# Kernel tuning notes

Hardware: AMD Instinct MI355X
Metric: run time of the kernel (lower is better)

## Reference

```python
import jax, jax.numpy as jnp
import numpy as np
import math

D_MODEL = 1024
NUM_HEADS = 16
D_FF = 4096
LN_EPS = 1e-5


def _layer_norm(x, gamma, beta):
    mu = jnp.mean(x, axis=-1, keepdims=True)
    var = jnp.mean(jnp.square(x - mu), axis=-1, keepdims=True)
    return (x - mu) / jnp.sqrt(var + LN_EPS) * gamma + beta


def setup_inputs() -> dict:
    key = jax.random.key(0)
    ks = jax.random.split(key, 16)
    S, B, D, F = 2048, 2, D_MODEL, D_FF
    sc = 0.02
    inp = {
        "x": jax.random.normal(ks[0], (S, B, D), dtype=jnp.float32),
        "Wq": jax.random.normal(ks[1], (D, D), dtype=jnp.float32) * sc,
        "bq": jnp.zeros((D,), jnp.float32),
        "Wk": jax.random.normal(ks[2], (D, D), dtype=jnp.float32) * sc,
        "bk": jnp.zeros((D,), jnp.float32),
        "Wv": jax.random.normal(ks[3], (D, D), dtype=jnp.float32) * sc,
        "bv": jnp.zeros((D,), jnp.float32),
        "Wo": jax.random.normal(ks[4], (D, D), dtype=jnp.float32) * sc,
        "bo": jnp.zeros((D,), jnp.float32),
        "g1": jnp.ones((D,), jnp.float32),
        "b1": jnp.zeros((D,), jnp.float32),
        "W1": jax.random.normal(ks[5], (D, F), dtype=jnp.float32) * sc,
        "bb1": jnp.zeros((F,), jnp.float32),
        "W2": jax.random.normal(ks[6], (F, D), dtype=jnp.float32) * sc,
        "bb2": jnp.zeros((D,), jnp.float32),
        "g2": jnp.ones((D,), jnp.float32),
        "b2": jnp.zeros((D,), jnp.float32),
    }
    return inp


def reference(x, Wq, bq, Wk, bk, Wv, bv, Wo, bo, g1, b1, W1, bb1, W2, bb2, g2, b2):
    # x: [S, B, D] (seq-first, matching the torch module)
    S, B, D = x.shape
    H = NUM_HEADS
    dh = D // H

    def split_(t):  # [S, B, D] -> [B*H, S, dh]  (same as view + transpose in torch)
        return jnp.swapaxes(t.reshape(S, B * H, dh), 0, 1)

    q = split_(x @ Wq + bq)
    k = split_(x @ Wk + bk)
    v = split_(x @ Wv + bv)

    # naive bmm -> softmax -> bmm attention (full [B*H, S, S] scores)
    scores = jnp.einsum("nsd,ntd->nst", q / math.sqrt(dh), k)
    attn = jax.nn.softmax(scores, axis=-1)
    o = jnp.einsum("nst,ntd->nsd", attn, v)  # [B*H, S, dh]
    o = jnp.swapaxes(o, 0, 1).reshape(S, B, D) @ Wo + bo

    x1 = _layer_norm(x + o, g1, b1)
    ff = jax.nn.relu(x1 @ W1 + bb1) @ W2 + bb2
    return _layer_norm(x1 + ff, g2, b2)
```

## Files before the change

### kernel.cpp

```cpp
#include <hip/hip_runtime.h>
#include <hip/hip_bf16.h>
#include <cstdint>

typedef __bf16 bf16_t;
typedef __attribute__((ext_vector_type(8))) __bf16 bf16x8;
typedef __attribute__((ext_vector_type(4))) __bf16 bf16x4;
typedef __attribute__((ext_vector_type(2))) __bf16 bf16x2;
typedef __attribute__((ext_vector_type(4))) float f32x4;

#define GLOBAL_AS __attribute__((address_space(1)))
#define LDS_AS __attribute__((address_space(3)))

__device__ __forceinline__ void lds_load16(void* lds, const void* g) {
    __builtin_amdgcn_global_load_lds((GLOBAL_AS void*)g, (LDS_AS void*)lds, 16, 0, 0);
}

__global__ __launch_bounds__(256) void prep_all(const float* __restrict__ x,
                                                const float* __restrict__ Wq,
                                                const float* __restrict__ Wk,
                                                const float* __restrict__ Wv,
                                                const float* __restrict__ Wo,
                                                const float* __restrict__ W1,
                                                const float* __restrict__ W2,
                                                const float* __restrict__ bq,
                                                const float* __restrict__ bk,
                                                const float* __restrict__ bv,
                                                bf16_t* __restrict__ xb,
                                                bf16_t* __restrict__ WqkvT,
                                                bf16_t* __restrict__ WoT,
                                                bf16_t* __restrict__ W1T,
                                                bf16_t* __restrict__ W2T,
                                                float* __restrict__ qkvb) {
    __shared__ float T[64][65];
    const int bid = blockIdx.x, tid = threadIdx.x;
    if (bid < 3072) {
        const float* W; bf16_t* WT; int Kd, Nd, lb;
        if (bid < 1024) {
            Kd = 1024; Nd = 1024; lb = bid & 255;
            const int w = bid >> 8;
            W  = (w == 0) ? Wq : (w == 1) ? Wk : (w == 2) ? Wv : Wo;
            WT = (w == 0) ? WqkvT : (w == 1) ? WqkvT + 1048576
               : (w == 2) ? WqkvT + 2097152 : WoT;
        } else if (bid < 2048) { W = W1; WT = W1T; Kd = 1024; Nd = 4096; lb = bid - 1024; }
        else                   { W = W2; WT = W2T; Kd = 4096; Nd = 1024; lb = bid - 2048; }
        const int nbk = Kd >> 6;
        const int bk = lb % nbk, bn = lb / nbk;
        const int k0 = bk << 6, n0 = bn << 6;
        #pragma unroll
        for (int rep = 0; rep < 4; ++rep) {
            int r = rep * 16 + (tid >> 4);
            int c = (tid & 15) * 4;
            float4 v = *(const float4*)(W + (size_t)(k0 + r) * Nd + n0 + c);
            T[r][c] = v.x; T[r][c + 1] = v.y; T[r][c + 2] = v.z; T[r][c + 3] = v.w;
        }
        __syncthreads();
        #pragma unroll
        for (int rep = 0; rep < 4; ++rep) {
            int r = rep * 16 + (tid >> 4);
            int c = (tid & 15) * 4;
            bf16x4 o;
            o[0] = (bf16_t)T[c][r]; o[1] = (bf16_t)T[c + 1][r];
            o[2] = (bf16_t)T[c + 2][r]; o[3] = (bf16_t)T[c + 3][r];
            *(bf16x4*)(WT + (size_t)(n0 + r) * Kd + k0 + c) = o;
        }
    } else if (bid < 7168) {
        const int i = (bid - 3072) * 256 + tid;
        float4 v = *(const float4*)(x + (size_t)i * 4);
        bf16x4 o;
        o[0] = (bf16_t)v.x; o[1] = (bf16_t)v.y; o[2] = (bf16_t)v.z; o[3] = (bf16_t)v.w;
        *(bf16x4*)(xb + (size_t)i * 4) = o;
    } else {
        const int i = (bid - 7168) * 256 + tid;
        if (i < 3072)
            qkvb[i] = (i < 1024) ? bq[i] : (i < 2048) ? bk[i - 1024] : bv[i - 2048];
    }
}

template <int OM, bool RELU>
__global__ __launch_bounds__(512, 2) void gemm256(const bf16_t* __restrict__ A,
                                                  const bf16_t* __restrict__ Bt,
                                                  const float* __restrict__ bias,
                                                  void* __restrict__ Cv,
                                                  int M, int N, int K,
                                                  int kc_len, int n_kc) {
    __shared__ alignas(16) bf16_t As[2][256 * 64];
    __shared__ alignas(16) bf16_t Bs[2][256 * 64];
    const int tid = threadIdx.x;
    const int wid = tid >> 6, lane = tid & 63;
    const int lr = lane & 15, lg = lane >> 4;
    const int wr = wid >> 2, wc = wid & 3;
    const int lrsw = (lr & 7) << 4;

    const int nbn = N >> 8;
    const int nbase = (M >> 8) * nbn;
    const int nwg = nbase * n_kc;
    int bid = blockIdx.x;
    int wg;
    if ((nwg & 7) == 0) { int q = nwg >> 3; wg = (bid & 7) * q + (bid >> 3); }
    else wg = bid;
    const int kc = wg / nbase;
    const int inner = wg - kc * nbase;
    const int bm = inner / nbn, bn = inner % nbn;

    f32x4 acc[8][4];
    #pragma unroll
    for (int i = 0; i < 8; ++i)
        #pragma unroll
        for (int j = 0; j < 4; ++j) acc[i][j] = f32x4{0.f, 0.f, 0.f, 0.f};

    const int srow = wid * 16 + (lane >> 3);
    const int colbyte = (((lane & 7) ^ (lane >> 3)) << 4);
    const char* gA = (const char*)(A + ((size_t)(bm * 256 + srow) * K + kc * kc_len)) + colbyte;
    const char* gB = (const char*)(Bt + ((size_t)(bn * 256 + srow) * K + kc * kc_len)) + colbyte;
    const size_t rs8 = (size_t)8 * K * 2;
    const size_t rs128 = (size_t)128 * K * 2;

    auto stA = [&](int b, int half, int kt) {
        char* d = (char*)As[b] + (half * 128 + wid * 16) * 128;
        const char* s = gA + (size_t)half * rs128 + (size_t)kt * 128;
        lds_load16(d, s);
        lds_load16(d + 1024, s + rs8);
    };
    auto stB = [&](int b, int half, int kt) {
        char* d = (char*)Bs[b] + (half * 128 + wid * 16) * 128;
        const char* s = gB + (size_t)half * rs128 + (size_t)kt * 128;
        lds_load16(d, s);
        lds_load16(d + 1024, s + rs8);
    };
    auto ldA = [&](int b, int m, int kk) {
        const int row = (m >> 2) * 128 + (m & 3) * 32 + wr * 16 + lr;
        return *(const bf16x8*)((const char*)As[b] + row * 128 + ((kk * 64 + lg * 16) ^ lrsw));
    };
    auto ldB = [&](int b, int n, int kk) {
        const int row = n * 64 + wc * 16 + lr;
        return *(const bf16x8*)((const char*)Bs[b] + row * 128 + ((kk * 64 + lg * 16) ^ lrsw));
    };

    const int NT = kc_len >> 6;
    stA(0, 0, 0); stB(0, 0, 0); stB(0, 1, 0); stA(0, 1, 0);
    asm volatile("s_waitcnt vmcnt(4)" ::: "memory");
    __builtin_amdgcn_s_barrier();

    bf16x8 afr[4][2], bfr[4][2];
    #pragma unroll 1
    for (int kt = 0; kt < NT; ++kt) {
        const int buf = kt & 1;
        const int ktn = (kt + 1 < NT) ? kt + 1 : kt;

        #pragma unroll
        for (int m = 0; m < 4; ++m) {
            afr[m][0] = ldA(buf, m, 0);
            afr[m][1] = ldA(buf, m, 1);
        }
        #pragma unroll
        for (int n = 0; n < 2; ++n) {
            bfr[n][0] = ldB(buf, n, 0);
            bfr[n][1] = ldB(buf, n, 1);
        }
        stA(buf ^ 1, 0, ktn);
        __builtin_amdgcn_s_barrier();
        __builtin_amdgcn_s_setprio(1);
        #pragma unroll
        for (int m = 0; m < 4; ++m)
            #pragma unroll
            for (int n = 0; n < 2; ++n) {
                acc[m][n] = __builtin_amdgcn_mfma_f32_16x16x32_bf16(afr[m][0], bfr[n][0], acc[m][n], 0, 0, 0);
                acc[m][n] = __builtin_amdgcn_mfma_f32_16x16x32_bf16(afr[m][1], bfr[n][1], acc[m][n], 0, 0, 0);
            }
        __builtin_amdgcn_s_setprio(0);
        asm volatile("s_waitcnt vmcnt(4)" ::: "memory");
        __builtin_amdgcn_s_barrier();

        #pragma unroll
        for (int n = 2; n < 4; ++n) {
            bfr[n][0] = ldB(buf, n, 0);
            bfr[n][1] = ldB(buf, n, 1);
        }
        stB(buf ^ 1, 0, ktn);
        __builtin_amdgcn_s_barrier();
        __builtin_amdgcn_s_setprio(1);
        #pragma unroll
        for (int m = 0; m < 4; ++m)
            #pragma unroll
            for (int n = 2; n < 4; ++n) {
                acc[m][n] = __builtin_amdgcn_mfma_f32_16x16x32_bf16(afr[m][0], bfr[n][0], acc[m][n], 0, 0, 0);
                acc[m][n] = __builtin_amdgcn_mfma_f32_16x16x32_bf16(afr[m][1], bfr[n][1], acc[m][n], 0, 0, 0);
            }
        __builtin_amdgcn_s_setprio(0);
        asm volatile("s_waitcnt vmcnt(4)" ::: "memory");
        __builtin_amdgcn_s_barrier();

        #pragma unroll
        for (int m = 0; m < 4; ++m) {
            afr[m][0] = ldA(buf, m + 4, 0);
            afr[m][1] = ldA(buf, m + 4, 1);
        }
        stB(buf ^ 1, 1, ktn);
        __builtin_amdgcn_s_barrier();
        __builtin_amdgcn_s_setprio(1);
        #pragma unroll
        for (int m = 0; m < 4; ++m)
            #pragma unroll
            for (int n = 0; n < 2; ++n) {
                acc[m + 4][n] = __builtin_amdgcn_mfma_f32_16x16x32_bf16(afr[m][0], bfr[n][0], acc[m + 4][n], 0, 0, 0);
                acc[m + 4][n] = __builtin_amdgcn_mfma_f32_16x16x32_bf16(afr[m][1], bfr[n][1], acc[m + 4][n], 0, 0, 0);
            }
        __builtin_amdgcn_s_setprio(0);
        __builtin_amdgcn_s_barrier();

        stA(buf ^ 1, 1, ktn);
        __builtin_amdgcn_s_barrier();
        __builtin_amdgcn_s_setprio(1);
        #pragma unroll
        for (int m = 0; m < 4; ++m)
            #pragma unroll
            for (int n = 2; n < 4; ++n) {
                acc[m + 4][n] = __builtin_amdgcn_mfma_f32_16x16x32_bf16(afr[m][0], bfr[n][0], acc[m + 4][n], 0, 0, 0);
                acc[m + 4][n] = __builtin_amdgcn_mfma_f32_16x16x32_bf16(afr[m][1], bfr[n][1], acc[m + 4][n], 0, 0, 0);
            }
        __builtin_amdgcn_s_setprio(0);
        asm volatile("s_waitcnt vmcnt(4)" ::: "memory");
        __builtin_amdgcn_s_barrier();
    }

    float* outf = (float*)Cv + (size_t)kc * M * N;
    bf16_t* outb = (bf16_t*)Cv + (size_t)kc * M * N;
    float bv[4];
    #pragma unroll
    for (int n = 0; n < 4; ++n) {
        const int c = (bn << 8) + n * 64 + wc * 16 + lr;
        bv[n] = (bias && kc == 0) ? bias[c] : 0.f;
    }
    #pragma unroll
    for (int m = 0; m < 8; ++m) {
        const int row0 = (bm << 8) + (m >> 2) * 128 + (m & 3) * 32 + wr * 16 + (lg << 2);
        #pragma unroll
        for (int n = 0; n < 4; ++n) {
            const int c = (bn << 8) + n * 64 + wc * 16 + lr;
            #pragma unroll
            for (int j = 0; j < 4; ++j) {
                float v = acc[m][n][j] + bv[n];
                if (RELU) v = fmaxf(v, 0.f);
                if (OM == 0)      ((bf16_t*)Cv)[(size_t)(row0 + j) * N + c] = (bf16_t)v;
                else if (OM == 1) outf[(size_t)(row0 + j) * N + c] = v;
                else              outb[(size_t)(row0 + j) * N + c] = (bf16_t)v;
            }
        }
    }
}

__global__ __launch_bounds__(256) void reshape_v(const bf16_t* __restrict__ QKV,
                                                 bf16_t* __restrict__ VT) {
    __shared__ alignas(16) bf16_t Vl[64][72];
    const int n = blockIdx.x >> 5, st = blockIdx.x & 31;
    const int b = n >> 4, h = n & 15;
    const int s0 = st << 6;
    const int tid = threadIdx.x;

    #pragma unroll
    for (int rep = 0; rep < 2; ++rep) {
        int chunk = rep * 256 + tid;
        int sl = chunk >> 3, c8 = (chunk & 7) << 3;
        size_t srow = (size_t)(s0 + sl) * 2 + b;
        *(bf16x8*)&Vl[sl][c8] = *(const bf16x8*)(QKV + srow * 3072 + 2048 + h * 64 + c8);
    }
    __syncthreads();
    #pragma unroll
    for (int rep = 0; rep < 2; ++rep) {
        int chunk = rep * 256 + tid;
        int d = chunk >> 3, c8 = (chunk & 7) << 3;
        bf16x8 v;
        #pragma unroll
        for (int e = 0; e < 8; ++e) v[e] = Vl[c8 + e][d];
        *(bf16x8*)(VT + ((size_t)n * 64 + d) * 2048 + s0 + c8) = v;
    }
}

__global__ __launch_bounds__(256) void attn_fwd(const bf16_t* __restrict__ QKV,
                                                const bf16_t* __restrict__ VT,
                                                bf16_t* __restrict__ O) {
    const int S = 2048;
    const int n = blockIdx.x >> 4;
    const int qt = blockIdx.x & 15;
    const int q0 = qt << 7;
    const int b = n >> 4, h = n & 15;
    const int tid = threadIdx.x, wid = tid >> 6, lane = tid & 63;
    const int lr = lane & 15, lg = lane >> 4;
    const int lrsw = (lr & 7) << 4;

    __shared__ alignas(16) bf16_t Ks[2][64 * 64];
    __shared__ alignas(16) bf16_t Vs[2][64 * 64];
    __shared__ alignas(16) bf16_t Ps[4][2][16 * 64];

    char* pbs0 = (char*)&Ps[wid][0][0];
    char* pbs1 = (char*)&Ps[wid][1][0];

    const float qsc = 0.125f * 1.4426950408889634f;
    auto scale8 = [&](bf16x8 v) {
        bf16x8 r;
        #pragma unroll
        for (int e = 0; e < 8; ++e) r[e] = (bf16_t)((float)v[e] * qsc);
        return r;
    };
    const bf16_t* Qrow0 = QKV + ((size_t)(q0 + wid * 32 + lr) * 2 + b) * 3072 + h * 64;
    const bf16_t* Qrow1 = Qrow0 + (size_t)16 * 2 * 3072;
    const bf16x8 qa0 = scale8(*(const bf16x8*)(Qrow0 + lg * 8));
    const bf16x8 qa1 = scale8(*(const bf16x8*)(Qrow0 + 32 + lg * 8));
    const bf16x8 qb0 = scale8(*(const bf16x8*)(Qrow1 + lg * 8));
    const bf16x8 qb1 = scale8(*(const bf16x8*)(Qrow1 + 32 + lg * 8));

    bf16x8 ones;
    #pragma unroll
    for (int e = 0; e < 8; ++e) ones[e] = (bf16_t)1.0f;

    const int colbyte = (((lane & 7) ^ (lane >> 3)) << 4);
    const size_t kstride = (size_t)2 * 3072 * 2;
    const char* ksrc0 = (const char*)QKV +
        (((size_t)(wid * 16 + (lane >> 3)) * 2 + b) * 3072 + 1024 + h * 64) * 2 + colbyte;
    const char* ksrc1 = ksrc0 + 8 * kstride;
    const char* vsrc0 = (const char*)(VT + ((size_t)n * 64 + wid * 16 + (lane >> 3)) * S) + colbyte;
    const char* vsrc1 = vsrc0 + (size_t)8 * S * 2;

    auto stage = [&](int bf, int t0) {
        lds_load16((char*)Ks[bf] + wid * 2048,        ksrc0 + (size_t)t0 * kstride);
        lds_load16((char*)Ks[bf] + wid * 2048 + 1024, ksrc1 + (size_t)t0 * kstride);
        lds_load16((char*)Vs[bf] + wid * 2048,        vsrc0 + (size_t)t0 * 2);
        lds_load16((char*)Vs[bf] + wid * 2048 + 1024, vsrc1 + (size_t)t0 * 2);
    };

    f32x4 oaccA[4], oaccB[4];
    #pragma unroll
    for (int i = 0; i < 4; ++i) {
        oaccA[i] = f32x4{0.f, 0.f, 0.f, 0.f};
        oaccB[i] = f32x4{0.f, 0.f, 0.f, 0.f};
    }
    f32x4 laccA = f32x4{0.f, 0.f, 0.f, 0.f};
    f32x4 laccB = f32x4{0.f, 0.f, 0.f, 0.f};

    stage(0, 0);
    int buf = 0;

    #pragma unroll 1
    for (int t0 = 0; t0 < S; t0 += 64) {
        if (t0 + 64 < S) {
            stage(buf ^ 1, t0 + 64);
            asm volatile("s_waitcnt vmcnt(4)" ::: "memory");
        } else {
            asm volatile("s_waitcnt vmcnt(0)" ::: "memory");
        }
        __builtin_amdgcn_s_barrier();

        const char* kb = (char*)Ks[buf];
        const char* vb = (char*)Vs[buf];

        f32x4 swA[4], swB[4];
        #pragma unroll
        for (int tc = 0; tc < 4; ++tc) {
            const char* krow = kb + (tc * 16 + lr) * 128;
            bf16x8 kf0 = *(const bf16x8*)(krow + ((lg * 16) ^ lrsw));
            bf16x8 kf1 = *(const bf16x8*)(krow + ((64 + lg * 16) ^ lrsw));
            f32x4 za = f32x4{-12.f, -12.f, -12.f, -12.f};
            za = __builtin_amdgcn_mfma_f32_16x16x32_bf16(kf0, qa0, za, 0, 0, 0);
            za = __builtin_amdgcn_mfma_f32_16x16x32_bf16(kf1, qa1, za, 0, 0, 0);
            swA[tc] = za;
            f32x4 zb = f32x4{-12.f, -12.f, -12.f, -12.f};
            zb = __builtin_amdgcn_mfma_f32_16x16x32_bf16(kf0, qb0, zb, 0, 0, 0);
            zb = __builtin_amdgcn_mfma_f32_16x16x32_bf16(kf1, qb1, zb, 0, 0, 0);
            swB[tc] = zb;
        }

        #pragma unroll
        for (int tc = 0; tc < 4; ++tc)
            #pragma unroll
            for (int j = 0; j < 4; ++j) {
                swA[tc][j] = __builtin_amdgcn_exp2f(swA[tc][j]);
                swB[tc][j] = __builtin_amdgcn_exp2f(swB[tc][j]);
            }

        #pragma unroll
        for (int tc = 0; tc < 4; ++tc)
            #pragma unroll
            for (int hh = 0; hh < 2; ++hh) {
                bf16x2 pa, pb;
                pa[0] = (bf16_t)swA[tc][2 * hh]; pa[1] = (bf16_t)swA[tc][2 * hh + 1];
                pb[0] = (bf16_t)swB[tc][2 * hh]; pb[1] = (bf16_t)swB[tc][2 * hh + 1];
                const int off = (tc * 32 + lg * 8 + hh * 4) ^ lrsw;
                *(bf16x2*)(pbs0 + lr * 128 + off) = pa;
                *(bf16x2*)(pbs1 + lr * 128 + off) = pb;
            }
        bf16x8 pA0 = *(const bf16x8*)(pbs0 + lr * 128 + ((lg * 16) ^ lrsw));
        bf16x8 pA1 = *(const bf16x8*)(pbs0 + lr * 128 + ((64 + lg * 16) ^ lrsw));
        bf16x8 pB0 = *(const bf16x8*)(pbs1 + lr * 128 + ((lg * 16) ^ lrsw));
        bf16x8 pB1 = *(const bf16x8*)(pbs1 + lr * 128 + ((64 + lg * 16) ^ lrsw));

        laccA = __builtin_amdgcn_mfma_f32_16x16x32_bf16(ones, pA0, laccA, 0, 0, 0);
        laccA = __builtin_amdgcn_mfma_f32_16x16x32_bf16(ones, pA1, laccA, 0, 0, 0);
        laccB = __builtin_amdgcn_mfma_f32_16x16x32_bf16(ones, pB0, laccB, 0, 0, 0);
        laccB = __builtin_amdgcn_mfma_f32_16x16x32_bf16(ones, pB1, laccB, 0, 0, 0);

        #pragma unroll
        for (int vc = 0; vc < 4; ++vc) {
            const char* vrow = vb + (vc * 16 + lr) * 128;
            bf16x8 vf0 = *(const bf16x8*)(vrow + ((lg * 16) ^ lrsw));
            bf16x8 vf1 = *(const bf16x8*)(vrow + ((64 + lg * 16) ^ lrsw));
            oaccA[vc] = __builtin_amdgcn_mfma_f32_16x16x32_bf16(vf0, pA0, oaccA[vc], 0, 0, 0);
            oaccA[vc] = __builtin_amdgcn_mfma_f32_16x16x32_bf16(vf1, pA1, oaccA[vc], 0, 0, 0);
            oaccB[vc] = __builtin_amdgcn_mfma_f32_16x16x32_bf16(vf0, pB0, oaccB[vc], 0, 0, 0);
            oaccB[vc] = __builtin_amdgcn_mfma_f32_16x16x32_bf16(vf1, pB1, oaccB[vc], 0, 0, 0);
        }
        __builtin_amdgcn_s_barrier();
        buf ^= 1;
    }

    const float invA = 1.0f / laccA[0];
    const float invB = 1.0f / laccB[0];
    const size_t tokA = (size_t)(q0 + wid * 32 + lr) * 2 + b;
    const size_t tokB = tokA + 32;
    #pragma unroll
    for (int vc = 0; vc < 4; ++vc) {
        bf16x4 oa, ob;
        #pragma unroll
        for (int j = 0; j < 4; ++j) {
            oa[j] = (bf16_t)(oaccA[vc][j] * invA);
            ob[j] = (bf16_t)(oaccB[vc][j] * invB);
        }
        *(bf16x4*)(O + tokA * 1024 + h * 64 + vc * 16 + lg * 4) = oa;
        *(bf16x4*)(O + tokB * 1024 + h * 64 + vc * 16 + lg * 4) = ob;
    }
}

template <int P>
__global__ __launch_bounds__(256) void ln_res(const float* __restrict__ X,
                                              const bf16_t* __restrict__ Y,
                                              const float* __restrict__ g,
                                              const float* __restrict__ be,
                                              float* __restrict__ outf,
                                              bf16_t* __restrict__ outb) {
    const int row = blockIdx.x, tid = threadIdx.x;
    const size_t base = (size_t)row * 1024 + tid * 4;
    const size_t pstride = (size_t)4096 * 1024;
    float4 xv = *(const float4*)(X + base);
    float v0 = xv.x, v1 = xv.y, v2 = xv.z, v3 = xv.w;
    #pragma unroll
    for (int p = 0; p < P; ++p) {
        bf16x4 yv = *(const bf16x4*)(Y + p * pstride + base);
        v0 += (float)yv[0]; v1 += (float)yv[1]; v2 += (float)yv[2]; v3 += (float)yv[3];
    }
    float s = v0 + v1 + v2 + v3;
    float sq = v0 * v0 + v1 * v1 + v2 * v2 + v3 * v3;
    #pragma unroll
    for (int m = 1; m < 64; m <<= 1) {
        s += __shfl_xor(s, m);
        sq += __shfl_xor(sq, m);
    }
    __shared__ float rs[4], rq[4];
    const int wid = tid >> 6;
    if ((tid & 63) == 0) { rs[wid] = s; rq[wid] = sq; }
    __syncthreads();
    s = rs[0] + rs[1] + rs[2] + rs[3];
    sq = rq[0] + rq[1] + rq[2] + rq[3];
    const float mu = s * (1.f / 1024.f);
    const float var = sq * (1.f / 1024.f) - mu * mu;
    const float rstd = rsqrtf(var + 1e-5f);
    float4 gv = *(const float4*)(g + tid * 4);
    float4 bv = *(const float4*)(be + tid * 4);
    float o0 = (v0 - mu) * rstd * gv.x + bv.x;
    float o1 = (v1 - mu) * rstd * gv.y + bv.y;
    float o2 = (v2 - mu) * rstd * gv.z + bv.z;
    float o3 = (v3 - mu) * rstd * gv.w + bv.w;
    float4 ov = {o0, o1, o2, o3};
    *(float4*)(outf + base) = ov;
    if (outb) {
        bf16x4 ob;
        ob[0] = (bf16_t)o0; ob[1] = (bf16_t)o1; ob[2] = (bf16_t)o2; ob[3] = (bf16_t)o3;
        *(bf16x4*)(outb + base) = ob;
    }
}

extern "C" void kernel_launch(void* const* d_in, const int* in_sizes, int n_in,
                              void* d_out, int out_size, void* d_ws, size_t ws_size,
                              hipStream_t stream) {
    (void)in_sizes; (void)n_in; (void)out_size; (void)ws_size;
    const float* x   = (const float*)d_in[0];
    const float* Wq  = (const float*)d_in[1];
    const float* bq  = (const float*)d_in[2];
    const float* Wk  = (const float*)d_in[3];
    const float* bk  = (const float*)d_in[4];
    const float* Wv  = (const float*)d_in[5];
    const float* bv  = (const float*)d_in[6];
    const float* Wo  = (const float*)d_in[7];
    const float* bo  = (const float*)d_in[8];
    const float* g1  = (const float*)d_in[9];
    const float* b1  = (const float*)d_in[10];
    const float* W1  = (const float*)d_in[11];
    const float* bb1 = (const float*)d_in[12];
    const float* W2  = (const float*)d_in[13];
    const float* bb2 = (const float*)d_in[14];
    const float* g2  = (const float*)d_in[15];
    const float* b2  = (const float*)d_in[16];
    float* out = (float*)d_out;

    char* ws = (char*)d_ws;
    const size_t MB = 1ull << 20;
    bf16_t* xb    = (bf16_t*)(ws + 0);
    bf16_t* WqkvT = (bf16_t*)(ws + 8 * MB);
    bf16_t* WoT   = (bf16_t*)(ws + 14 * MB);
    bf16_t* W1T   = (bf16_t*)(ws + 16 * MB);
    bf16_t* W2T   = (bf16_t*)(ws + 24 * MB);
    float*  qkvb  = (float*)(ws + 32 * MB);
    bf16_t* QKV   = (bf16_t*)(ws + 33 * MB);
    bf16_t* VTh   = (bf16_t*)(ws + 57 * MB);
    bf16_t* Otok  = (bf16_t*)(ws + 65 * MB);
    bf16_t* WoP   = (bf16_t*)(ws + 73 * MB);
    float*  x1f   = (float*)(ws + 105 * MB);
    bf16_t* x1b   = (bf16_t*)(ws + 121 * MB);
    bf16_t* Hff   = (bf16_t*)(ws + 129 * MB);
    bf16_t* W2P   = (bf16_t*)(ws + 33 * MB);

    prep_all<<<7180, 256, 0, stream>>>(x, Wq, Wk, Wv, Wo, W1, W2, bq, bk, bv,
                                       xb, WqkvT, WoT, W1T, W2T, qkvb);

    gemm256<0, false><<<192, 512, 0, stream>>>(xb, WqkvT, qkvb, QKV, 4096, 3072, 1024, 1024, 1);
    reshape_v<<<1024, 256, 0, stream>>>(QKV, VTh);
    attn_fwd<<<512, 256, 0, stream>>>(QKV, VTh, Otok);
    gemm256<2, false><<<256, 512, 0, stream>>>(Otok, WoT, bo, WoP, 4096, 1024, 1024, 256, 4);
    ln_res<4><<<4096, 256, 0, stream>>>(x, WoP, g1, b1, x1f, x1b);

    gemm256<0, true><<<256, 512, 0, stream>>>(x1b, W1T, bb1, Hff, 4096, 4096, 1024, 1024, 1);
    gemm256<2, false><<<256, 512, 0, stream>>>(Hff, W2T, bb2, W2P, 4096, 1024, 4096, 1024, 4);
    ln_res<4><<<4096, 256, 0, stream>>>(x1f, W2P, g2, b2, out, nullptr);
}
```

Baseline: 230.6 us.

## Triple-buffer attention K/V staging, widen P stores, use bf16 residuals in layernorm

The attention loop moves from double to triple buffering of K/V tiles in LDS, which removes one barrier per iteration and issues each prefetch two tiles ahead. The P tile is now written to LDS with bf16x4 stores instead of bf16x2, halving the store count. Both residual layernorm passes read the residual as bf16 (xb and x1b) instead of fp32, and the fp32 x1 intermediate is no longer written. This cuts memory traffic but lowers residual precision, and the redundant restaging of the last tile adds some wasted loads.

```diff
diff --git a/kernel.cpp b/kernel.cpp
--- a/kernel.cpp
+++ b/kernel.cpp
@@ -288,8 +288,8 @@
     const int lr = lane & 15, lg = lane >> 4;
     const int lrsw = (lr & 7) << 4;
 
-    __shared__ alignas(16) bf16_t Ks[2][64 * 64];
-    __shared__ alignas(16) bf16_t Vs[2][64 * 64];
+    __shared__ alignas(16) bf16_t Ks[3][64 * 64];
+    __shared__ alignas(16) bf16_t Vs[3][64 * 64];
     __shared__ alignas(16) bf16_t Ps[4][2][16 * 64];
 
     char* pbs0 = (char*)&Ps[wid][0][0];
@@ -338,20 +338,17 @@
     f32x4 laccB = f32x4{0.f, 0.f, 0.f, 0.f};
 
     stage(0, 0);
-    int buf = 0;
+    stage(1, 64);
 
     #pragma unroll 1
-    for (int t0 = 0; t0 < S; t0 += 64) {
-        if (t0 + 64 < S) {
-            stage(buf ^ 1, t0 + 64);
-            asm volatile("s_waitcnt vmcnt(4)" ::: "memory");
-        } else {
-            asm volatile("s_waitcnt vmcnt(0)" ::: "memory");
-        }
-        __builtin_amdgcn_s_barrier();
-
-        const char* kb = (char*)Ks[buf];
-        const char* vb = (char*)Vs[buf];
+    for (int t = 0; t < 32; ++t) {
+        asm volatile("s_waitcnt vmcnt(4)" ::: "memory");
+        __builtin_amdgcn_s_barrier();
+        const int tn = (t + 2 < 32) ? t + 2 : 31;
+        stage((t + 2) % 3, tn * 64);
+
+        const char* kb = (char*)Ks[t % 3];
+        const char* vb = (char*)Vs[t % 3];
 
         f32x4 swA[4], swB[4];
         #pragma unroll
@@ -378,16 +375,16 @@
             }
 
         #pragma unroll
-        for (int tc = 0; tc < 4; ++tc)
-            #pragma unroll
-            for (int hh = 0; hh < 2; ++hh) {
-                bf16x2 pa, pb;
-                pa[0] = (bf16_t)swA[tc][2 * hh]; pa[1] = (bf16_t)swA[tc][2 * hh + 1];
-                pb[0] = (bf16_t)swB[tc][2 * hh]; pb[1] = (bf16_t)swB[tc][2 * hh + 1];
-                const int off = (tc * 32 + lg * 8 + hh * 4) ^ lrsw;
-                *(bf16x2*)(pbs0 + lr * 128 + off) = pa;
-                *(bf16x2*)(pbs1 + lr * 128 + off) = pb;
-            }
+        for (int tc = 0; tc < 4; ++tc) {
+            bf16x4 pa, pb;
+            pa[0] = (bf16_t)swA[tc][0]; pa[1] = (bf16_t)swA[tc][1];
+            pa[2] = (bf16_t)swA[tc][2]; pa[3] = (bf16_t)swA[tc][3];
+            pb[0] = (bf16_t)swB[tc][0]; pb[1] = (bf16_t)swB[tc][1];
+            pb[2] = (bf16_t)swB[tc][2]; pb[3] = (bf16_t)swB[tc][3];
+            const int off = (tc * 32 + lg * 8) ^ lrsw;
+            *(bf16x4*)(pbs0 + lr * 128 + off) = pa;
+            *(bf16x4*)(pbs1 + lr * 128 + off) = pb;
+        }
         bf16x8 pA0 = *(const bf16x8*)(pbs0 + lr * 128 + ((lg * 16) ^ lrsw));
         bf16x8 pA1 = *(const bf16x8*)(pbs0 + lr * 128 + ((64 + lg * 16) ^ lrsw));
         bf16x8 pB0 = *(const bf16x8*)(pbs1 + lr * 128 + ((lg * 16) ^ lrsw));
@@ -408,8 +405,6 @@
             oaccB[vc] = __builtin_amdgcn_mfma_f32_16x16x32_bf16(vf0, pB0, oaccB[vc], 0, 0, 0);
             oaccB[vc] = __builtin_amdgcn_mfma_f32_16x16x32_bf16(vf1, pB1, oaccB[vc], 0, 0, 0);
         }
-        __builtin_amdgcn_s_barrier();
-        buf ^= 1;
     }
 
     const float invA = 1.0f / laccA[0];
@@ -430,7 +425,7 @@
 }
 
 template <int P>
-__global__ __launch_bounds__(256) void ln_res(const float* __restrict__ X,
+__global__ __launch_bounds__(256) void ln_res(const bf16_t* __restrict__ X,
                                               const bf16_t* __restrict__ Y,
                                               const float* __restrict__ g,
                                               const float* __restrict__ be,
@@ -439,8 +434,8 @@
     const int row = blockIdx.x, tid = threadIdx.x;
     const size_t base = (size_t)row * 1024 + tid * 4;
     const size_t pstride = (size_t)4096 * 1024;
-    float4 xv = *(const float4*)(X + base);
-    float v0 = xv.x, v1 = xv.y, v2 = xv.z, v3 = xv.w;
+    bf16x4 xv = *(const bf16x4*)(X + base);
+    float v0 = (float)xv[0], v1 = (float)xv[1], v2 = (float)xv[2], v3 = (float)xv[3];
     #pragma unroll
     for (int p = 0; p < P; ++p) {
         bf16x4 yv = *(const bf16x4*)(Y + p * pstride + base);
@@ -468,8 +463,10 @@
     float o1 = (v1 - mu) * rstd * gv.y + bv.y;
     float o2 = (v2 - mu) * rstd * gv.z + bv.z;
     float o3 = (v3 - mu) * rstd * gv.w + bv.w;
-    float4 ov = {o0, o1, o2, o3};
-    *(float4*)(outf + base) = ov;
+    if (outf) {
+        float4 ov = {o0, o1, o2, o3};
+        *(float4*)(outf + base) = ov;
+    }
     if (outb) {
         bf16x4 ob;
         ob[0] = (bf16_t)o0; ob[1] = (bf16_t)o1; ob[2] = (bf16_t)o2; ob[3] = (bf16_t)o3;
@@ -512,9 +509,8 @@
     bf16_t* VTh   = (bf16_t*)(ws + 57 * MB);
     bf16_t* Otok  = (bf16_t*)(ws + 65 * MB);
     bf16_t* WoP   = (bf16_t*)(ws + 73 * MB);
-    float*  x1f   = (float*)(ws + 105 * MB);
-    bf16_t* x1b   = (bf16_t*)(ws + 121 * MB);
-    bf16_t* Hff   = (bf16_t*)(ws + 129 * MB);
+    bf16_t* x1b   = (bf16_t*)(ws + 105 * MB);
+    bf16_t* Hff   = (bf16_t*)(ws + 113 * MB);
     bf16_t* W2P   = (bf16_t*)(ws + 33 * MB);
 
     prep_all<<<7180, 256, 0, stream>>>(x, Wq, Wk, Wv, Wo, W1, W2, bq, bk, bv,
@@ -524,9 +520,9 @@
     reshape_v<<<1024, 256, 0, stream>>>(QKV, VTh);
     attn_fwd<<<512, 256, 0, stream>>>(QKV, VTh, Otok);
     gemm256<2, false><<<256, 512, 0, stream>>>(Otok, WoT, bo, WoP, 4096, 1024, 1024, 256, 4);
-    ln_res<4><<<4096, 256, 0, stream>>>(x, WoP, g1, b1, x1f, x1b);
+    ln_res<4><<<4096, 256, 0, stream>>>(xb, WoP, g1, b1, nullptr, x1b);
 
     gemm256<0, true><<<256, 512, 0, stream>>>(x1b, W1T, bb1, Hff, 4096, 4096, 1024, 1024, 1);
     gemm256<2, false><<<256, 512, 0, stream>>>(Hff, W2T, bb2, W2P, 4096, 1024, 4096, 1024, 4);
-    ln_res<4><<<4096, 256, 0, stream>>>(x1f, W2P, g2, b2, out, nullptr);
-}
+    ln_res<4><<<4096, 256, 0, stream>>>(x1b, W2P, g2, b2, out, nullptr);
+}
```

New measurement: 240.8 us. +4.4%, slower.
